# Performance work log

Hardware: AMD Instinct MI355X
Metric: run time of the kernel (lower is better)

Reference implementation:

```python
import jax, jax.numpy as jnp
import numpy as np

NUM_USERS = 60000
NUM_ITEMS = 40000
N_NODES = NUM_USERS + NUM_ITEMS
EMBED_K = 128
E_HALF = 1_000_000  # bipartite interactions; symmetrized -> 2M directed edges


def setup_inputs() -> dict:
    key = jax.random.key(0)
    k1, k2, k3, k4, k5, k6, k7 = jax.random.split(key, 7)
    scale = 1.0 / np.sqrt(EMBED_K)  # ~ xavier_normal
    Gu = jax.random.normal(k1, (NUM_USERS, EMBED_K), jnp.float32) * scale
    Gi = jax.random.normal(k2, (NUM_ITEMS, EMBED_K), jnp.float32) * scale
    W0 = jax.random.normal(k3, (EMBED_K, EMBED_K), jnp.float32) * scale
    W1 = jax.random.normal(k4, (EMBED_K, EMBED_K), jnp.float32) * scale
    W2 = jax.random.normal(k5, (EMBED_K, EMBED_K), jnp.float32) * scale
    # bipartite user-item graph, symmetrized (items offset by NUM_USERS)
    u = jax.random.randint(k6, (E_HALF,), 0, NUM_USERS)
    it = jax.random.randint(k7, (E_HALF,), 0, NUM_ITEMS) + NUM_USERS
    src = jnp.concatenate([u, it])
    dst = jnp.concatenate([it, u])
    edge_index = jnp.stack([src, dst]).astype(jnp.int32)  # [2, 2M]
    return {"Gu": Gu, "Gi": Gi, "W0": W0, "W1": W1, "W2": W2,
            "edge_index": edge_index}


def reference(Gu, Gi, W0, W1, W2, edge_index):
    # add_self_loops=False, bias=False) -> ReLU), then split into (gu, gi).
    src, dst = edge_index[0], edge_index[1]
    n_users = Gu.shape[0]
    n_nodes = Gu.shape[0] + Gi.shape[0]
    # PyG gcn_norm (no self loops): deg = scatter(1, col); norm = d^-1/2[row]*d^-1/2[col]
    ones = jnp.ones(src.shape, Gu.dtype)
    deg = jax.ops.segment_sum(ones, dst, num_segments=n_nodes)
    dinv = jnp.where(deg > 0, jax.lax.rsqrt(jnp.maximum(deg, 1.0)), 0.0)
    norm = dinv[src] * dinv[dst]  # [E]
    x = jnp.concatenate([Gu, Gi], axis=0)  # [N, d]
    for W in (W0, W1, W2):
        h = x @ W                                   # [N, d] dense GEMM
        msg = h[src] * norm[:, None]                # [E, d] gather + scale
        x = jax.nn.relu(jax.ops.segment_sum(msg, dst, num_segments=n_nodes))
    return x[:n_users], x[n_users:]
```

## Files before the change

kernel.cpp:

```cpp
#include <hip/hip_runtime.h>
#include <hip/hip_bf16.h>

#define EMB 128
#define NPB 256
#define NB_PAD 512
#define CHUNK 4096

typedef unsigned int uint32;

__device__ __forceinline__ ushort f2bf(float f) {
    uint32 u = __float_as_uint(f);
    return (ushort)((u + 0x7fff + ((u >> 16) & 1)) >> 16);
}


__global__ __launch_bounds__(256) void bucket_count_kernel(
    const int* __restrict__ dst, int* __restrict__ bucket_cnt, int E, int NB) {
    __shared__ int cnt[NB_PAD];
    int t = threadIdx.x;
    long e0 = (long)blockIdx.x * CHUNK;
    int n = E - (int)e0; if (n > CHUNK) n = CHUNK;
    for (int b = t; b < NB_PAD; b += 256) cnt[b] = 0;
    __syncthreads();
    #pragma unroll
    for (int i = 0; i < CHUNK / 256; i++) {
        int idx = t + i * 256;
        if (idx < n) atomicAdd(&cnt[dst[e0 + idx] >> 8], 1);
    }
    __syncthreads();
    for (int b = t; b < NB; b += 256)
        if (cnt[b] > 0) atomicAdd(&bucket_cnt[b], cnt[b]);
}

__global__ void bucket_scan_kernel(const int* __restrict__ bucket_cnt,
                                   int* __restrict__ ebase, int* __restrict__ gcursor,
                                   int NB, int E) {
    __shared__ int sc[512];
    int t = threadIdx.x;
    int v = (t < NB) ? bucket_cnt[t] : 0;
    sc[t] = v;
    __syncthreads();
    for (int off = 1; off < 512; off <<= 1) {
        int u = (t >= off) ? sc[t - off] : 0;
        __syncthreads();
        sc[t] += u;
        __syncthreads();
    }
    if (t < NB) {
        int excl = sc[t] - v;
        ebase[t] = excl;
        gcursor[t] = excl;
    }
    if (t == 0) ebase[NB] = E;
}


__global__ __launch_bounds__(256) void bucket_scatter_kernel(
    const int* __restrict__ src, const int* __restrict__ dst,
    int* __restrict__ gcursor, uint2* __restrict__ ebuf, int E, int NB) {
    __shared__ int cnt[NB_PAD];
    __shared__ int loff[NB_PAD];
    __shared__ int gbase[NB_PAD];
    __shared__ int pos[NB_PAD];
    __shared__ int sc[256];
    __shared__ uint2 stage[CHUNK];
    int t = threadIdx.x;
    long e0 = (long)blockIdx.x * CHUNK;
    int n = E - (int)e0; if (n > CHUNK) n = CHUNK;
    for (int b = t; b < NB_PAD; b += 256) { cnt[b] = 0; pos[b] = 0; }
    __syncthreads();
    int es[CHUNK / 256], ed[CHUNK / 256];
    #pragma unroll
    for (int i = 0; i < CHUNK / 256; i++) {
        int idx = t + i * 256;
        if (idx < n) {
            es[i] = src[e0 + idx];
            ed[i] = dst[e0 + idx];
            atomicAdd(&cnt[ed[i] >> 8], 1);
        }
    }
    __syncthreads();
    int a = cnt[2 * t], b2 = cnt[2 * t + 1];
    sc[t] = a + b2;
    __syncthreads();
    for (int off = 1; off < 256; off <<= 1) {
        int v = (t >= off) ? sc[t - off] : 0;
        __syncthreads();
        sc[t] += v;
        __syncthreads();
    }
    int excl = sc[t] - (a + b2);
    loff[2 * t] = excl;
    loff[2 * t + 1] = excl + a;
    __syncthreads();
    for (int b = t; b < NB; b += 256)
        if (cnt[b] > 0) gbase[b] = atomicAdd(&gcursor[b], cnt[b]);
    __syncthreads();
    #pragma unroll
    for (int i = 0; i < CHUNK / 256; i++) {
        int idx = t + i * 256;
        if (idx < n) {
            int b = ed[i] >> 8;
            int p = atomicAdd(&pos[b], 1);
            stage[loff[b] + p] = make_uint2((uint32)es[i], (uint32)ed[i]);
        }
    }
    __syncthreads();
    for (int b = t; b < NB; b += 256) {
        int c = cnt[b], lo = loff[b], go = gbase[b];
        for (int k = 0; k < c; k++) ebuf[go + k] = stage[lo + k];
    }
}


__global__ __launch_bounds__(256) void bucket_deg_kernel(
    const uint2* __restrict__ ebuf, const int* __restrict__ ebase,
    int* __restrict__ deg, float* __restrict__ dinv, int N) {
    __shared__ int cnt[NPB];
    int t = threadIdx.x;
    int n0 = blockIdx.x * NPB;
    int nn = N - n0; if (nn > NPB) nn = NPB;
    cnt[t] = 0;
    __syncthreads();
    int e0 = ebase[blockIdx.x];
    int e1 = ebase[blockIdx.x + 1];
    for (int e = e0 + t; e < e1; e += 256) {
        uint2 sd = ebuf[e];
        atomicAdd(&cnt[(int)sd.y - n0], 1);
    }
    __syncthreads();
    if (t < nn) {
        int c = cnt[t];
        deg[n0 + t] = c;
        dinv[n0 + t] = c > 0 ? rsqrtf((float)c) : 0.0f;
    }
}


__global__ void scan1_kernel(const int* __restrict__ deg, int* __restrict__ rowptr,
                             int* __restrict__ bsum, int N) {
    __shared__ int sc[256];
    int t = threadIdx.x;
    int base = blockIdx.x * 1024 + t * 4;
    int d0 = 0, d1 = 0, d2 = 0, d3 = 0;
    if (base + 3 < N) {
        int4 v = *(const int4*)(deg + base);
        d0 = v.x; d1 = v.y; d2 = v.z; d3 = v.w;
    } else {
        if (base     < N) d0 = deg[base];
        if (base + 1 < N) d1 = deg[base + 1];
        if (base + 2 < N) d2 = deg[base + 2];
        if (base + 3 < N) d3 = deg[base + 3];
    }
    int s = d0 + d1 + d2 + d3;
    sc[t] = s;
    __syncthreads();
    for (int off = 1; off < 256; off <<= 1) {
        int v = (t >= off) ? sc[t - off] : 0;
        __syncthreads();
        sc[t] += v;
        __syncthreads();
    }
    int excl = sc[t] - s;
    if (t == 255) bsum[blockIdx.x] = sc[255];
    int dd[4] = {d0, d1, d2, d3};
    int p = excl;
    #pragma unroll
    for (int j = 0; j < 4; j++) {
        int i = base + j;
        if (i < N) rowptr[i] = p;
        p += dd[j];
    }
}

__global__ void scan2_kernel(int* bsum, int nb) {
    __shared__ int sc[128];
    int t = threadIdx.x;
    int v = (t < nb) ? bsum[t] : 0;
    sc[t] = v;
    __syncthreads();
    for (int off = 1; off < 128; off <<= 1) {
        int u = (t >= off) ? sc[t - off] : 0;
        __syncthreads();
        sc[t] += u;
        __syncthreads();
    }
    if (t < nb) bsum[t] = sc[t] - v;
}

__global__ void scan3_kernel(int* __restrict__ rowptr, const int* __restrict__ bsum,
                             int N, int E) {
    int t = threadIdx.x, b = blockIdx.x;
    int add = bsum[b];
    int base = b * 1024 + t * 4;
    #pragma unroll
    for (int j = 0; j < 4; j++) {
        int i = base + j;
        if (i < N) rowptr[i] += add;
    }
    if (b == 0 && t == 0) rowptr[N] = E;
}


__global__ __launch_bounds__(256) void bucket_fill_kernel(
    const uint2* __restrict__ ebuf, const int* __restrict__ rowptr,
    int* __restrict__ csr, int N) {
    __shared__ int cnt[NPB];
    __shared__ int rp[NPB];
    int t = threadIdx.x;
    int n0 = blockIdx.x * NPB;
    int nn = N - n0; if (nn > NPB) nn = NPB;
    if (t < nn) { cnt[t] = 0; rp[t] = rowptr[n0 + t]; }
    __syncthreads();
    int e0 = rowptr[n0];
    int e1 = rowptr[n0 + nn];
    for (int e = e0 + t; e < e1; e += 256) {
        uint2 sd = ebuf[e];
        int local = (int)sd.y - n0;
        int p = atomicAdd(&cnt[local], 1);
        csr[rp[local] + p] = (int)sd.x;
    }
}


__global__ __launch_bounds__(256) void agg_relu_kernel(
    const uint32* __restrict__ Yh,
    const int* __restrict__ rowptr, const int* __restrict__ csr,
    const float* __restrict__ dinv, float* __restrict__ out, int N) {
    int node = blockIdx.x * 4 + (threadIdx.x >> 6);
    int lane = threadIdx.x & 63;
    if (node >= N) return;
    int e0 = rowptr[node], e1 = rowptr[node + 1];
    float ax = 0.0f, ay = 0.0f;
    for (int base = e0; base < e1; base += 64) {
        int n = e1 - base;
        if (n > 64) n = 64;
        int s = 0;
        float w = 0.0f;
        if (lane < n) {
            s = csr[base + lane];
            w = dinv[s];
        }
        int nn = (n + 15) & ~15;
        for (int j = 0; j < nn; j += 16) {
            uint32 p[16];
            float wj[16];
            #pragma unroll
            for (int u = 0; u < 16; u++) {
                int sj = __shfl(s, j + u);
                wj[u] = __shfl(w, j + u);
                p[u] = Yh[(size_t)sj * 64 + lane];
            }
            #pragma unroll
            for (int u = 0; u < 16; u++) {
                ax += wj[u] * __uint_as_float(p[u] << 16);
                ay += wj[u] * __uint_as_float(p[u] & 0xffff0000u);
            }
        }
    }
    float wd = dinv[node];
    float2 r;
    r.x = fmaxf(ax * wd, 0.0f);
    r.y = fmaxf(ay * wd, 0.0f);
    *(float2*)(out + (size_t)node * EMB + lane * 2) = r;
}


__global__ __launch_bounds__(256) void gemm_kernel(
    const float* __restrict__ A, const float* __restrict__ W,
    ushort* __restrict__ Yh, int M) {
    __shared__ float As[64][36];
    __shared__ float Ws[32][128];
    int t = threadIdx.x;
    int row0 = blockIdx.x * 64;
    int cg = t & 15, rg = t >> 4;
    int c0 = cg * 4;
    float4 acc0[4] = {};
    float4 acc1[4] = {};
    for (int k0 = 0; k0 < 128; k0 += 32) {
        int f = t;
        #pragma unroll
        for (int it = 0; it < 2; it++, f += 256) {
            int r = f >> 3, kk4 = (f & 7) * 4;
            int row = row0 + r;
            float4 v = {0.f, 0.f, 0.f, 0.f};
            if (row < M) v = *(const float4*)(A + (size_t)row * EMB + k0 + kk4);
            *(float4*)&As[r][kk4] = v;
        }
        int g = t;
        #pragma unroll
        for (int it = 0; it < 4; it++, g += 256) {
            int kk = g >> 5, c4 = (g & 31) * 4;
            *(float4*)&Ws[kk][c4] = *(const float4*)(W + (size_t)(k0 + kk) * EMB + c4);
        }
        __syncthreads();
        #pragma unroll
        for (int kk4 = 0; kk4 < 32; kk4 += 4) {
            float4 a[4];
            #pragma unroll
            for (int r = 0; r < 4; r++) a[r] = *(const float4*)&As[rg * 4 + r][kk4];
            #pragma unroll
            for (int kk = 0; kk < 4; kk++) {
                float4 w0 = *(const float4*)&Ws[kk4 + kk][c0];
                float4 w1 = *(const float4*)&Ws[kk4 + kk][64 + c0];
                #pragma unroll
                for (int r = 0; r < 4; r++) {
                    float av = (kk == 0) ? a[r].x : (kk == 1) ? a[r].y
                             : (kk == 2) ? a[r].z : a[r].w;
                    acc0[r].x += av * w0.x; acc0[r].y += av * w0.y;
                    acc0[r].z += av * w0.z; acc0[r].w += av * w0.w;
                    acc1[r].x += av * w1.x; acc1[r].y += av * w1.y;
                    acc1[r].z += av * w1.z; acc1[r].w += av * w1.w;
                }
            }
        }
        __syncthreads();
    }
    #pragma unroll
    for (int r = 0; r < 4; r++) {
        int row = row0 + rg * 4 + r;
        if (row < M) {
            float4 v0 = acc0[r], v1 = acc1[r];
            ushort4 h0, h1;
            h0.x = f2bf(v0.x); h0.y = f2bf(v0.y); h0.z = f2bf(v0.z); h0.w = f2bf(v0.w);
            h1.x = f2bf(v1.x); h1.y = f2bf(v1.y); h1.z = f2bf(v1.z); h1.w = f2bf(v1.w);
            *(ushort4*)(Yh + (size_t)row * EMB + c0) = h0;
            *(ushort4*)(Yh + (size_t)row * EMB + 64 + c0) = h1;
        }
    }
}


extern "C" void kernel_launch(void* const* d_in, const int* in_sizes, int n_in,
                              void* d_out, int out_size, void* d_ws, size_t ws_size,
                              hipStream_t stream) {
    (void)n_in; (void)out_size; (void)ws_size;
    const float* Gu = (const float*)d_in[0];
    const float* Gi = (const float*)d_in[1];
    const float* W0 = (const float*)d_in[2];
    const float* W1 = (const float*)d_in[3];
    const float* W2 = (const float*)d_in[4];
    const int* ei = (const int*)d_in[5];

    int nu = in_sizes[0] / EMB;
    int ni = in_sizes[1] / EMB;
    int N = nu + ni;
    int E = in_sizes[5] / 2;
    const int* src = ei;
    const int* dst = ei + E;
    int NB = (N + NPB - 1) / NPB;

    ushort* Yh      = (ushort*)d_ws;
    uint2* ebuf     = (uint2*)(Yh + (size_t)N * EMB);
    int* deg        = (int*)(ebuf + (size_t)E);
    int* rowptr     = deg + N;
    float* dinv     = (float*)(rowptr + N + 1);
    int* csr        = (int*)(dinv + N);
    int* bucket_cnt = csr + E;
    int* ebase      = bucket_cnt + NB;
    int* gcursor    = ebase + NB + 1;
    int* bsum       = gcursor + NB;
    float* X        = (float*)d_out;

    hipMemsetAsync(bucket_cnt, 0, sizeof(int) * (size_t)NB, stream);

    int ecb = (E + CHUNK - 1) / CHUNK;
    bucket_count_kernel<<<ecb, 256, 0, stream>>>(dst, bucket_cnt, E, NB);
    bucket_scan_kernel<<<1, 512, 0, stream>>>(bucket_cnt, ebase, gcursor, NB, E);
    bucket_scatter_kernel<<<ecb, 256, 0, stream>>>(src, dst, gcursor, ebuf, E, NB);
    bucket_deg_kernel<<<NB, 256, 0, stream>>>(ebuf, ebase, deg, dinv, N);
    int nb = (N + 1023) / 1024;
    scan1_kernel<<<nb, 256, 0, stream>>>(deg, rowptr, bsum, N);
    scan2_kernel<<<1, 128, 0, stream>>>(bsum, nb);
    scan3_kernel<<<nb, 256, 0, stream>>>(rowptr, bsum, N, E);
    bucket_fill_kernel<<<NB, 256, 0, stream>>>(ebuf, rowptr, csr, N);

    int aggBlocks = (N + 3) / 4;

    gemm_kernel<<<(nu + 63) / 64, 256, 0, stream>>>(Gu, W0, Yh, nu);
    gemm_kernel<<<(ni + 63) / 64, 256, 0, stream>>>(Gi, W0, Yh + (size_t)nu * EMB, ni);
    agg_relu_kernel<<<aggBlocks, 256, 0, stream>>>((const uint32*)Yh, rowptr, csr, dinv, X, N);
    gemm_kernel<<<(N + 63) / 64, 256, 0, stream>>>(X, W1, Yh, N);
    agg_relu_kernel<<<aggBlocks, 256, 0, stream>>>((const uint32*)Yh, rowptr, csr, dinv, X, N);
    gemm_kernel<<<(N + 63) / 64, 256, 0, stream>>>(X, W2, Yh, N);
    agg_relu_kernel<<<aggBlocks, 256, 0, stream>>>((const uint32*)Yh, rowptr, csr, dinv, X, N);
}
```

Measured before the change: 498.2 us.

## Replace FP32 SIMT GEMM with split-bf16 MFMA GEMM using register-resident weights

Replaces the scalar FP32 tiled GEMM with a persistent MFMA kernel that emulates FP32 precision using hi/lo bf16 splits (three bf16 MFMA products per tile). A new pre-kernel splits and transposes the three weight matrices into hi/lo bf16 once per launch, and each wave keeps its weight fragments in registers across all row tiles. The goal is to offload the dense transforms to matrix cores. The cost is extra split arithmetic on activations and slightly lower precision than true FP32, while the sparse aggregation, which probably dominates, is left unchanged.

```diff
diff --git a/kernel.cpp b/kernel.cpp
--- a/kernel.cpp
+++ b/kernel.cpp
@@ -7,10 +7,15 @@
 #define CHUNK 4096
 
 typedef unsigned int uint32;
+typedef __attribute__((ext_vector_type(8))) short bf16x8;
+typedef __attribute__((ext_vector_type(4))) float f32x4;
 
 __device__ __forceinline__ ushort f2bf(float f) {
     uint32 u = __float_as_uint(f);
     return (ushort)((u + 0x7fff + ((u >> 16) & 1)) >> 16);
+}
+__device__ __forceinline__ uint32 pack_hi2(uint32 u0, uint32 u1) {
+    return (u1 & 0xffff0000u) | (u0 >> 16);
 }
 
 
@@ -266,66 +271,122 @@
 }
 
 
-__global__ __launch_bounds__(256) void gemm_kernel(
-    const float* __restrict__ A, const float* __restrict__ W,
-    ushort* __restrict__ Yh, int M) {
-    __shared__ float As[64][36];
-    __shared__ float Ws[32][128];
-    int t = threadIdx.x;
-    int row0 = blockIdx.x * 64;
-    int cg = t & 15, rg = t >> 4;
-    int c0 = cg * 4;
-    float4 acc0[4] = {};
-    float4 acc1[4] = {};
-    for (int k0 = 0; k0 < 128; k0 += 32) {
-        int f = t;
-        #pragma unroll
-        for (int it = 0; it < 2; it++, f += 256) {
-            int r = f >> 3, kk4 = (f & 7) * 4;
-            int row = row0 + r;
-            float4 v = {0.f, 0.f, 0.f, 0.f};
-            if (row < M) v = *(const float4*)(A + (size_t)row * EMB + k0 + kk4);
-            *(float4*)&As[r][kk4] = v;
-        }
-        int g = t;
-        #pragma unroll
-        for (int it = 0; it < 4; it++, g += 256) {
-            int kk = g >> 5, c4 = (g & 31) * 4;
-            *(float4*)&Ws[kk][c4] = *(const float4*)(W + (size_t)(k0 + kk) * EMB + c4);
-        }
-        __syncthreads();
-        #pragma unroll
-        for (int kk4 = 0; kk4 < 32; kk4 += 4) {
-            float4 a[4];
-            #pragma unroll
-            for (int r = 0; r < 4; r++) a[r] = *(const float4*)&As[rg * 4 + r][kk4];
-            #pragma unroll
-            for (int kk = 0; kk < 4; kk++) {
-                float4 w0 = *(const float4*)&Ws[kk4 + kk][c0];
-                float4 w1 = *(const float4*)&Ws[kk4 + kk][64 + c0];
-                #pragma unroll
-                for (int r = 0; r < 4; r++) {
-                    float av = (kk == 0) ? a[r].x : (kk == 1) ? a[r].y
-                             : (kk == 2) ? a[r].z : a[r].w;
-                    acc0[r].x += av * w0.x; acc0[r].y += av * w0.y;
-                    acc0[r].z += av * w0.z; acc0[r].w += av * w0.w;
-                    acc1[r].x += av * w1.x; acc1[r].y += av * w1.y;
-                    acc1[r].z += av * w1.z; acc1[r].w += av * w1.w;
-                }
+__global__ void wsplit_kernel(const float* __restrict__ W0, const float* __restrict__ W1,
+                              const float* __restrict__ W2,
+                              ushort* __restrict__ Whi, ushort* __restrict__ Wlo) {
+    const float* W = (blockIdx.x == 0) ? W0 : (blockIdx.x == 1) ? W1 : W2;
+    ushort* hiT = Whi + blockIdx.x * EMB * EMB;
+    ushort* loT = Wlo + blockIdx.x * EMB * EMB;
+    for (int i = threadIdx.x; i < EMB * EMB; i += blockDim.x) {
+        int k = i >> 7, n = i & 127;
+        float w = W[i];
+        uint32 u = __float_as_uint(w);
+        ushort hi = (ushort)(u >> 16);
+        float hif = __uint_as_float(u & 0xffff0000u);
+        ushort lo = f2bf(w - hif);
+        hiT[n * EMB + k] = hi;
+        loT[n * EMB + k] = lo;
+    }
+}
+
+
+union FragU { uint32 u[4]; bf16x8 v; };
+
+__global__ __launch_bounds__(256, 2) void gemm_mfma_kernel(
+    const float* __restrict__ A, const ushort* __restrict__ WhiT,
+    const ushort* __restrict__ WloT, ushort* __restrict__ Yh, int M) {
+    __shared__ float As[16][132];
+    int t = threadIdx.x;
+    int wv = t >> 6, lane = t & 63, quad = lane >> 4, l16 = lane & 15;
+
+    FragU bfr[8][2];
+    #pragma unroll
+    for (int kc = 0; kc < 8; kc++) {
+        const ushort* srcW = (kc < 4) ? WhiT : WloT;
+        int kb = (kc & 3) * 32 + quad * 8;
+        #pragma unroll
+        for (int c = 0; c < 2; c++) {
+            int n = wv * 32 + c * 16 + l16;
+            const uint32* p = (const uint32*)(srcW + n * EMB + kb);
+            bfr[kc][c].u[0] = p[0];
+            bfr[kc][c].u[1] = p[1];
+            bfr[kc][c].u[2] = p[2];
+            bfr[kc][c].u[3] = p[3];
+        }
+    }
+
+    int srow = t >> 4, skq = t & 15;
+    int ntile = (M + 15) >> 4;
+    for (int tile = blockIdx.x; tile < ntile; tile += (int)gridDim.x) {
+        int r0 = tile << 4;
+        __syncthreads();
+        {
+            float4 v0 = {0.f, 0.f, 0.f, 0.f}, v1 = v0;
+            int row = r0 + srow;
+            if (row < M) {
+                const float* ga = A + (size_t)row * EMB + skq * 8;
+                v0 = *(const float4*)ga;
+                v1 = *(const float4*)(ga + 4);
             }
-        }
-        __syncthreads();
-    }
-    #pragma unroll
-    for (int r = 0; r < 4; r++) {
-        int row = row0 + rg * 4 + r;
-        if (row < M) {
-            float4 v0 = acc0[r], v1 = acc1[r];
-            ushort4 h0, h1;
-            h0.x = f2bf(v0.x); h0.y = f2bf(v0.y); h0.z = f2bf(v0.z); h0.w = f2bf(v0.w);
-            h1.x = f2bf(v1.x); h1.y = f2bf(v1.y); h1.z = f2bf(v1.z); h1.w = f2bf(v1.w);
-            *(ushort4*)(Yh + (size_t)row * EMB + c0) = h0;
-            *(ushort4*)(Yh + (size_t)row * EMB + 64 + c0) = h1;
+            *(float4*)&As[srow][skq * 8] = v0;
+            *(float4*)&As[srow][skq * 8 + 4] = v1;
+        }
+        __syncthreads();
+
+        FragU ah[4], al[4];
+        #pragma unroll
+        for (int kc = 0; kc < 4; kc++) {
+            const float* p = &As[l16][kc * 32 + quad * 8];
+            float4 xa = *(const float4*)p;
+            float4 xb = *(const float4*)(p + 4);
+            uint32 u0 = __float_as_uint(xa.x), u1 = __float_as_uint(xa.y);
+            uint32 u2 = __float_as_uint(xa.z), u3 = __float_as_uint(xa.w);
+            uint32 u4 = __float_as_uint(xb.x), u5 = __float_as_uint(xb.y);
+            uint32 u6 = __float_as_uint(xb.z), u7 = __float_as_uint(xb.w);
+            ah[kc].u[0] = pack_hi2(u0, u1);
+            ah[kc].u[1] = pack_hi2(u2, u3);
+            ah[kc].u[2] = pack_hi2(u4, u5);
+            ah[kc].u[3] = pack_hi2(u6, u7);
+            float l0 = xa.x - __uint_as_float(u0 & 0xffff0000u);
+            float l1 = xa.y - __uint_as_float(u1 & 0xffff0000u);
+            float l2 = xa.z - __uint_as_float(u2 & 0xffff0000u);
+            float l3 = xa.w - __uint_as_float(u3 & 0xffff0000u);
+            float l4 = xb.x - __uint_as_float(u4 & 0xffff0000u);
+            float l5 = xb.y - __uint_as_float(u5 & 0xffff0000u);
+            float l6 = xb.z - __uint_as_float(u6 & 0xffff0000u);
+            float l7 = xb.w - __uint_as_float(u7 & 0xffff0000u);
+            al[kc].u[0] = pack_hi2(__float_as_uint(l0), __float_as_uint(l1));
+            al[kc].u[1] = pack_hi2(__float_as_uint(l2), __float_as_uint(l3));
+            al[kc].u[2] = pack_hi2(__float_as_uint(l4), __float_as_uint(l5));
+            al[kc].u[3] = pack_hi2(__float_as_uint(l6), __float_as_uint(l7));
+        }
+
+        f32x4 acc0 = {0.f, 0.f, 0.f, 0.f};
+        f32x4 acc1 = {0.f, 0.f, 0.f, 0.f};
+        #pragma unroll
+        for (int kc = 0; kc < 4; kc++) {
+            acc0 = __builtin_amdgcn_mfma_f32_16x16x32_bf16(ah[kc].v, bfr[kc][0].v, acc0, 0, 0, 0);
+            acc1 = __builtin_amdgcn_mfma_f32_16x16x32_bf16(ah[kc].v, bfr[kc][1].v, acc1, 0, 0, 0);
+        }
+        #pragma unroll
+        for (int kc = 0; kc < 4; kc++) {
+            acc0 = __builtin_amdgcn_mfma_f32_16x16x32_bf16(ah[kc].v, bfr[kc + 4][0].v, acc0, 0, 0, 0);
+            acc1 = __builtin_amdgcn_mfma_f32_16x16x32_bf16(ah[kc].v, bfr[kc + 4][1].v, acc1, 0, 0, 0);
+        }
+        #pragma unroll
+        for (int kc = 0; kc < 4; kc++) {
+            acc0 = __builtin_amdgcn_mfma_f32_16x16x32_bf16(al[kc].v, bfr[kc][0].v, acc0, 0, 0, 0);
+            acc1 = __builtin_amdgcn_mfma_f32_16x16x32_bf16(al[kc].v, bfr[kc][1].v, acc1, 0, 0, 0);
+        }
+
+        int colb = wv * 32 + l16;
+        #pragma unroll
+        for (int r = 0; r < 4; r++) {
+            int row = r0 + quad * 4 + r;
+            if (row < M) {
+                Yh[(size_t)row * EMB + colb]      = f2bf(acc0[r]);
+                Yh[(size_t)row * EMB + colb + 16] = f2bf(acc1[r]);
+            }
         }
     }
 }
@@ -360,9 +421,13 @@
     int* ebase      = bucket_cnt + NB;
     int* gcursor    = ebase + NB + 1;
     int* bsum       = gcursor + NB;
+    ushort* WhiT    = (ushort*)(bsum + 128);
+    ushort* WloT    = WhiT + 3 * EMB * EMB;
     float* X        = (float*)d_out;
 
     hipMemsetAsync(bucket_cnt, 0, sizeof(int) * (size_t)NB, stream);
+
+    wsplit_kernel<<<3, 256, 0, stream>>>(W0, W1, W2, WhiT, WloT);
 
     int ecb = (E + CHUNK - 1) / CHUNK;
     bucket_count_kernel<<<ecb, 256, 0, stream>>>(dst, bucket_cnt, E, NB);
@@ -376,12 +441,13 @@
     bucket_fill_kernel<<<NB, 256, 0, stream>>>(ebuf, rowptr, csr, N);
 
     int aggBlocks = (N + 3) / 4;
-
-    gemm_kernel<<<(nu + 63) / 64, 256, 0, stream>>>(Gu, W0, Yh, nu);
-    gemm_kernel<<<(ni + 63) / 64, 256, 0, stream>>>(Gi, W0, Yh + (size_t)nu * EMB, ni);
+    const int GB = 512;
+
+    gemm_mfma_kernel<<<GB, 256, 0, stream>>>(Gu, WhiT, WloT, Yh, nu);
+    gemm_mfma_kernel<<<GB, 256, 0, stream>>>(Gi, WhiT, WloT, Yh + (size_t)nu * EMB, ni);
     agg_relu_kernel<<<aggBlocks, 256, 0, stream>>>((const uint32*)Yh, rowptr, csr, dinv, X, N);
-    gemm_kernel<<<(N + 63) / 64, 256, 0, stream>>>(X, W1, Yh, N);
+    gemm_mfma_kernel<<<GB, 256, 0, stream>>>(X, WhiT + EMB * EMB, WloT + EMB * EMB, Yh, N);
     agg_relu_kernel<<<aggBlocks, 256, 0, stream>>>((const uint32*)Yh, rowptr, csr, dinv, X, N);
-    gemm_kernel<<<(N + 63) / 64, 256, 0, stream>>>(X, W2, Yh, N);
+    gemm_mfma_kernel<<<GB, 256, 0, stream>>>(X, WhiT + 2 * EMB * EMB, WloT + 2 * EMB * EMB, Yh, N);
     agg_relu_kernel<<<aggBlocks, 256, 0, stream>>>((const uint32*)Yh, rowptr, csr, dinv, X, N);
 }
```

Result: faster. 470.5 us (-5.6%).
